# Optimization experiments

Measured on AMD Instinct MI355X. Metric: run time of the kernel, lower is better.

The kernel has to match this reference:

```python
import jax, jax.numpy as jnp
import numpy as np
from jax import lax


def _box_conv3d(x, win):
    k = jnp.ones((1, 1, win, win, win), x.dtype) / float(win ** 3)
    pad = win // 2
    return lax.conv_general_dilated(
        x, k,
        window_strides=(1, 1, 1),
        padding=[(pad, pad)] * 3,
        dimension_numbers=('NCDHW', 'OIDHW', 'NCDHW'),
    )


def setup_inputs() -> dict:
    key = jax.random.key(0)
    k1, k2 = jax.random.split(key)
    shape = (1, 1, 160, 192, 224)
    pred = jax.random.uniform(k1, shape, dtype=jnp.float32)
    target = jax.random.uniform(k2, shape, dtype=jnp.float32)
    return {'pred': pred, 'target': target, 'window_size': 9}


def reference(pred, target, window_size):
    Ii = target
    Ji = pred
    win = window_size
    mu1 = _box_conv3d(Ii, win)
    mu2 = _box_conv3d(Ji, win)
    mu1_sq = mu1 * mu1
    mu2_sq = mu2 * mu2
    mu1_mu2 = mu1 * mu2
    sigma1_sq = _box_conv3d(Ii * Ii, win) - mu1_sq
    sigma2_sq = _box_conv3d(Ji * Ji, win) - mu2_sq
    sigma12 = _box_conv3d(Ii * Ji, win) - mu1_mu2
    eps = jnp.finfo(sigma12.dtype).eps
    cc = sigma12 * sigma12 / jnp.maximum(sigma1_sq * sigma2_sq, eps)
    return -jnp.mean(cc)
```

## Files before the change

kernel.cpp:

```cpp
#include <hip/hip_runtime.h>
#include <hip/hip_fp16.h>

#define D_  160
#define H_  192
#define W_  224
#define HW_ (H_ * W_)
#define HW2_ (HW_ / 2)
#define N_  (D_ * H_ * W_)
#define INV729 (1.0f / 729.0f)
#define HSEG 16
#define NSEG (H_ / HSEG)
#define NROW (HSEG + 9)
#define UPD  (NSEG * 2)


__device__ __forceinline__ unsigned pack2(float a, float b) {
    const __half2 h = __floats2half2_rn(a, b);
    return *(const unsigned*)&h;
}

__global__ __launch_bounds__(64) void k_passWH(const float* __restrict__ pred,
                                               const float* __restrict__ targ,
                                               uint4* __restrict__ outA,
                                               unsigned* __restrict__ outB,
                                               double* __restrict__ acc) {
    if (blockIdx.x == 0 && threadIdx.x == 0) *acc = 0.0;

    const int lane = threadIdx.x;
    const int unit = blockIdx.x;
    const int d    = unit / UPD;
    const int rem  = unit % UPD;
    const int half = rem & 1;
    const int h0   = (rem >> 1) * HSEG;
    const long dbase = (long)d * HW_;
    const int wbase = half * 112;
    const int w0    = wbase + 2 * lane;

    if (lane < 56) {
        int coff[5];
        #pragma unroll
        for (int m = 0; m < 5; ++m) {
            const int wc = w0 - 4 + 2 * m;
            coff[m] = wc < 0 ? 0 : (wc > W_ - 2 ? W_ - 2 : wc);
        }
        bool vm[10];
        #pragma unroll
        for (int k = 0; k < 10; ++k) {
            const int wk = w0 - 4 + k;
            vm[k] = (wk >= 0) && (wk < W_);
        }

        float2 q[5][9];
        #pragma unroll
        for (int c = 0; c < 5; ++c)
            #pragma unroll
            for (int k = 0; k < 9; ++k) q[c][k] = make_float2(0.f, 0.f);
        float S0[5] = {0,0,0,0,0}, S1[5] = {0,0,0,0,0};

        const float* baseI = targ + dbase;
        const float* baseJ = pred + dbase;

        #pragma unroll
        for (int p = 0; p < NROW; ++p) {
            const int hh = h0 - 5 + p;
            float x[10], y[10];
            if (hh >= 0 && hh < H_) {
                const float* rI = baseI + (long)hh * W_;
                const float* rJ = baseJ + (long)hh * W_;
                #pragma unroll
                for (int m = 0; m < 5; ++m) {
                    const float2 vI = *(const float2*)(rI + coff[m]);
                    const float2 vJ = *(const float2*)(rJ + coff[m]);
                    x[2*m] = vI.x; x[2*m+1] = vI.y;
                    y[2*m] = vJ.x; y[2*m+1] = vJ.y;
                }
                #pragma unroll
                for (int k = 0; k < 10; ++k) {
                    if (k != 4 && k != 5) {
                        x[k] = vm[k] ? x[k] : 0.f;
                        y[k] = vm[k] ? y[k] : 0.f;
                    }
                }
            } else {
                #pragma unroll
                for (int k = 0; k < 10; ++k) { x[k] = 0.f; y[k] = 0.f; }
            }

            float sI = 0.f, sJ = 0.f, sII = 0.f, sJJ = 0.f, sIJ = 0.f;
            #pragma unroll
            for (int kk = 0; kk < 9; ++kk) {
                sI  += x[kk];          sJ  += y[kk];
                sII = fmaf(x[kk], x[kk], sII);
                sJJ = fmaf(y[kk], y[kk], sJJ);
                sIJ = fmaf(x[kk], y[kk], sIJ);
            }
            float w0s[5], w1s[5];
            w0s[0] = sI;  w1s[0] = sI  + x[9] - x[0];
            w0s[1] = sJ;  w1s[1] = sJ  + y[9] - y[0];
            w0s[2] = sII; w1s[2] = sII + x[9]*x[9] - x[0]*x[0];
            w0s[3] = sJJ; w1s[3] = sJJ + y[9]*y[9] - y[0]*y[0];
            w0s[4] = sIJ; w1s[4] = sIJ + x[9]*y[9] - x[0]*y[0];

            const int ph = p % 9;
            #pragma unroll
            for (int c = 0; c < 5; ++c) {
                S0[c] += w0s[c] - q[c][ph].x;
                S1[c] += w1s[c] - q[c][ph].y;
                q[c][ph].x = w0s[c];
                q[c][ph].y = w1s[c];
            }
            if (p >= 9) {
                const long rb = dbase + (long)(h0 + p - 9) * W_;
                uint4 oA;
                oA.x = pack2(S0[0], S0[1]); oA.y = pack2(S0[2], S0[3]);
                oA.z = pack2(S1[0], S1[1]); oA.w = pack2(S1[2], S1[3]);
                outA[rb / 2 + half * 56 + lane] = oA;
                outB[rb / 2 + half * 56 + lane] = pack2(S0[4], S1[4]);
            }
        }
    }
}

__global__ __launch_bounds__(256) void k_passD(const uint4* __restrict__ bufA,
                                               const unsigned* __restrict__ bufB,
                                               double* __restrict__ acc) {
    const int DSEG = D_ / 8;
    const int p2 = blockIdx.x * blockDim.x + threadIdx.x;
    const int d0 = blockIdx.y * DSEG;

    float2 q[5][9], S[5];
    #pragma unroll
    for (int c = 0; c < 5; ++c) S[c] = make_float2(0.f, 0.f);

    #pragma unroll
    for (int k = 0; k < 9; ++k) {
        const int dd = d0 - 5 + k;
        uint4 va = make_uint4(0u, 0u, 0u, 0u);
        unsigned vb = 0u;
        if (dd >= 0) {
            va = bufA[(long)dd * HW2_ + p2];
            vb = bufB[(long)dd * HW2_ + p2];
        }
        const float2 a01 = __half22float2(*(const __half2*)&va.x);
        const float2 a23 = __half22float2(*(const __half2*)&va.y);
        const float2 b01 = __half22float2(*(const __half2*)&va.z);
        const float2 b23 = __half22float2(*(const __half2*)&va.w);
        const float2 c44 = __half22float2(*(const __half2*)&vb);
        q[0][k] = make_float2(a01.x, b01.x); S[0].x += a01.x; S[0].y += b01.x;
        q[1][k] = make_float2(a01.y, b01.y); S[1].x += a01.y; S[1].y += b01.y;
        q[2][k] = make_float2(a23.x, b23.x); S[2].x += a23.x; S[2].y += b23.x;
        q[3][k] = make_float2(a23.y, b23.y); S[3].x += a23.y; S[3].y += b23.y;
        q[4][k] = make_float2(c44.x, c44.y); S[4].x += c44.x; S[4].y += c44.y;
    }

    float myacc = 0.f;
    #pragma unroll
    for (int j = 0; j < DSEG; ++j) {
        const int dd = d0 + 4 + j;
        uint4 va = make_uint4(0u, 0u, 0u, 0u);
        unsigned vb = 0u;
        if (dd < D_) {
            va = bufA[(long)dd * HW2_ + p2];
            vb = bufB[(long)dd * HW2_ + p2];
        }
        const float2 a01 = __half22float2(*(const __half2*)&va.x);
        const float2 a23 = __half22float2(*(const __half2*)&va.y);
        const float2 b01 = __half22float2(*(const __half2*)&va.z);
        const float2 b23 = __half22float2(*(const __half2*)&va.w);
        const float2 c44 = __half22float2(*(const __half2*)&vb);
        const float2 nv[5] = {
            make_float2(a01.x, b01.x), make_float2(a01.y, b01.y),
            make_float2(a23.x, b23.x), make_float2(a23.y, b23.y),
            make_float2(c44.x, c44.y)
        };
        const int ph = j % 9;
        #pragma unroll
        for (int c = 0; c < 5; ++c) {
            S[c].x += nv[c].x - q[c][ph].x;
            S[c].y += nv[c].y - q[c][ph].y;
            q[c][ph] = nv[c];
        }
        #pragma unroll
        for (int e = 0; e < 2; ++e) {
            const float mu1 = (e ? S[0].y : S[0].x) * INV729;
            const float mu2 = (e ? S[1].y : S[1].x) * INV729;
            const float s1  = (e ? S[2].y : S[2].x) * INV729 - mu1 * mu1;
            const float s2  = (e ? S[3].y : S[3].x) * INV729 - mu2 * mu2;
            const float s12 = (e ? S[4].y : S[4].x) * INV729 - mu1 * mu2;
            const float den = fmaxf(s1 * s2, 1.1920929e-7f);
            myacc += (s12 * s12) / den;
        }
    }

    __shared__ float red[256];
    red[threadIdx.x] = myacc;
    __syncthreads();
    #pragma unroll
    for (int s = 128; s > 0; s >>= 1) {
        if (threadIdx.x < s) red[threadIdx.x] += red[threadIdx.x + s];
        __syncthreads();
    }
    if (threadIdx.x == 0) atomicAdd(acc, (double)red[0]);
}

__global__ void k_fin(const double* __restrict__ acc, float* __restrict__ out) {
    out[0] = (float)(-(*acc) / (double)N_);
}

extern "C" void kernel_launch(void* const* d_in, const int* in_sizes, int n_in,
                              void* d_out, int out_size, void* d_ws, size_t ws_size,
                              hipStream_t stream) {
    const float* pred = (const float*)d_in[0];
    const float* targ = (const float*)d_in[1];

    uint4*    bufA = (uint4*)d_ws;
    unsigned* bufB = (unsigned*)((char*)d_ws + (size_t)(N_ / 2) * 16);
    double*   acc  = (double*)((char*)d_ws + (size_t)(N_ / 2) * 16 + (size_t)(N_ / 2) * 4);
    float*    out  = (float*)d_out;

    k_passWH<<<D_ * UPD, 64, 0, stream>>>(pred, targ, bufA, bufB, acc);
    dim3 g3(HW2_ / 256, 8);
    k_passD<<<g3, 256, 0, stream>>>(bufA, bufB, acc);
    k_fin<<<1, 1, 0, stream>>>(acc, out);
}
```

Baseline: 62.23 us.

## Split fused W/H box-filter pass into separate W and H kernels

Result: slower. 73.96 us (+18.8%).

```diff
diff --git a/kernel.cpp b/kernel.cpp
--- a/kernel.cpp
+++ b/kernel.cpp
@@ -7,11 +7,8 @@
 #define HW_ (H_ * W_)
 #define HW2_ (HW_ / 2)
 #define N_  (D_ * H_ * W_)
+#define NP2 (N_ / 2)
 #define INV729 (1.0f / 729.0f)
-#define HSEG 16
-#define NSEG (H_ / HSEG)
-#define NROW (HSEG + 9)
-#define UPD  (NSEG * 2)
 
 
 __device__ __forceinline__ unsigned pack2(float a, float b) {
@@ -19,105 +16,127 @@
     return *(const unsigned*)&h;
 }
 
-__global__ __launch_bounds__(64) void k_passWH(const float* __restrict__ pred,
+__global__ __launch_bounds__(256) void k_passW(const float* __restrict__ pred,
                                                const float* __restrict__ targ,
                                                uint4* __restrict__ outA,
                                                unsigned* __restrict__ outB,
                                                double* __restrict__ acc) {
     if (blockIdx.x == 0 && threadIdx.x == 0) *acc = 0.0;
-
-    const int lane = threadIdx.x;
-    const int unit = blockIdx.x;
-    const int d    = unit / UPD;
-    const int rem  = unit % UPD;
-    const int half = rem & 1;
-    const int h0   = (rem >> 1) * HSEG;
-    const long dbase = (long)d * HW_;
-    const int wbase = half * 112;
-    const int w0    = wbase + 2 * lane;
-
-    if (lane < 56) {
-        int coff[5];
+    const int pp = blockIdx.x * 256 + threadIdx.x;
+    const int row = pp / 112;
+    const int ri  = pp % 112;
+    const int w0  = 2 * ri;
+    const float* rI = targ + (long)row * W_;
+    const float* rJ = pred + (long)row * W_;
+
+    float x[10], y[10];
+    #pragma unroll
+    for (int m = 0; m < 5; ++m) {
+        const int wc  = w0 - 4 + 2 * m;
+        const int wcc = wc < 0 ? 0 : (wc > W_ - 2 ? W_ - 2 : wc);
+        const float2 vI = *(const float2*)(rI + wcc);
+        const float2 vJ = *(const float2*)(rJ + wcc);
+        x[2*m] = vI.x; x[2*m+1] = vI.y;
+        y[2*m] = vJ.x; y[2*m+1] = vJ.y;
+    }
+    #pragma unroll
+    for (int k = 0; k < 10; ++k) {
+        if (k != 4 && k != 5) {
+            const int wk = w0 - 4 + k;
+            const bool v = (wk >= 0) && (wk < W_);
+            x[k] = v ? x[k] : 0.f;
+            y[k] = v ? y[k] : 0.f;
+        }
+    }
+    float sI = 0.f, sJ = 0.f, sII = 0.f, sJJ = 0.f, sIJ = 0.f;
+    #pragma unroll
+    for (int kk = 0; kk < 9; ++kk) {
+        sI += x[kk]; sJ += y[kk];
+        sII = fmaf(x[kk], x[kk], sII);
+        sJJ = fmaf(y[kk], y[kk], sJJ);
+        sIJ = fmaf(x[kk], y[kk], sIJ);
+    }
+    const float tI  = sI  + x[9] - x[0];
+    const float tJ  = sJ  + y[9] - y[0];
+    const float tII = sII + x[9]*x[9] - x[0]*x[0];
+    const float tJJ = sJJ + y[9]*y[9] - y[0]*y[0];
+    const float tIJ = sIJ + x[9]*y[9] - x[0]*y[0];
+
+    uint4 oA;
+    oA.x = pack2(sI, sJ);  oA.y = pack2(sII, sJJ);
+    oA.z = pack2(tI, tJ);  oA.w = pack2(tII, tJJ);
+    outA[pp] = oA;
+    outB[pp] = pack2(sIJ, tIJ);
+}
+
+__global__ __launch_bounds__(256) void k_passH2(const uint4* __restrict__ inA,
+                                                const unsigned* __restrict__ inB,
+                                                uint4* __restrict__ outA,
+                                                unsigned* __restrict__ outB) {
+    const int HSEG2 = H_ / 8;
+    const int cc = blockIdx.x * blockDim.x + threadIdx.x;
+    const int d  = cc / 112;
+    const int ri = cc % 112;
+    const int h0 = blockIdx.y * HSEG2;
+    const long colbase = (long)d * HW2_ + ri;
+
+    float2 q[5][9], S[5];
+    #pragma unroll
+    for (int c = 0; c < 5; ++c) S[c] = make_float2(0.f, 0.f);
+
+    #pragma unroll
+    for (int k = 0; k < 9; ++k) {
+        const int hh = h0 - 5 + k;
+        uint4 va = make_uint4(0u, 0u, 0u, 0u);
+        unsigned vb = 0u;
+        if (hh >= 0) {
+            va = inA[colbase + (long)hh * 112];
+            vb = inB[colbase + (long)hh * 112];
+        }
+        const float2 f01 = __half22float2(*(const __half2*)&va.x);
+        const float2 f23 = __half22float2(*(const __half2*)&va.y);
+        const float2 g01 = __half22float2(*(const __half2*)&va.z);
+        const float2 g23 = __half22float2(*(const __half2*)&va.w);
+        const float2 c44 = __half22float2(*(const __half2*)&vb);
+        q[0][k] = make_float2(f01.x, g01.x); S[0].x += f01.x; S[0].y += g01.x;
+        q[1][k] = make_float2(f01.y, g01.y); S[1].x += f01.y; S[1].y += g01.y;
+        q[2][k] = make_float2(f23.x, g23.x); S[2].x += f23.x; S[2].y += g23.x;
+        q[3][k] = make_float2(f23.y, g23.y); S[3].x += f23.y; S[3].y += g23.y;
+        q[4][k] = make_float2(c44.x, c44.y); S[4].x += c44.x; S[4].y += c44.y;
+    }
+
+    #pragma unroll
+    for (int j = 0; j < HSEG2; ++j) {
+        const int hh = h0 + 4 + j;
+        uint4 va = make_uint4(0u, 0u, 0u, 0u);
+        unsigned vb = 0u;
+        if (hh < H_) {
+            va = inA[colbase + (long)hh * 112];
+            vb = inB[colbase + (long)hh * 112];
+        }
+        const float2 f01 = __half22float2(*(const __half2*)&va.x);
+        const float2 f23 = __half22float2(*(const __half2*)&va.y);
+        const float2 g01 = __half22float2(*(const __half2*)&va.z);
+        const float2 g23 = __half22float2(*(const __half2*)&va.w);
+        const float2 c44 = __half22float2(*(const __half2*)&vb);
+        const float2 nv[5] = {
+            make_float2(f01.x, g01.x), make_float2(f01.y, g01.y),
+            make_float2(f23.x, g23.x), make_float2(f23.y, g23.y),
+            make_float2(c44.x, c44.y)
+        };
+        const int ph = j % 9;
         #pragma unroll
-        for (int m = 0; m < 5; ++m) {
-            const int wc = w0 - 4 + 2 * m;
-            coff[m] = wc < 0 ? 0 : (wc > W_ - 2 ? W_ - 2 : wc);
-        }
-        bool vm[10];
-        #pragma unroll
-        for (int k = 0; k < 10; ++k) {
-            const int wk = w0 - 4 + k;
-            vm[k] = (wk >= 0) && (wk < W_);
-        }
-
-        float2 q[5][9];
-        #pragma unroll
-        for (int c = 0; c < 5; ++c)
-            #pragma unroll
-            for (int k = 0; k < 9; ++k) q[c][k] = make_float2(0.f, 0.f);
-        float S0[5] = {0,0,0,0,0}, S1[5] = {0,0,0,0,0};
-
-        const float* baseI = targ + dbase;
-        const float* baseJ = pred + dbase;
-
-        #pragma unroll
-        for (int p = 0; p < NROW; ++p) {
-            const int hh = h0 - 5 + p;
-            float x[10], y[10];
-            if (hh >= 0 && hh < H_) {
-                const float* rI = baseI + (long)hh * W_;
-                const float* rJ = baseJ + (long)hh * W_;
-                #pragma unroll
-                for (int m = 0; m < 5; ++m) {
-                    const float2 vI = *(const float2*)(rI + coff[m]);
-                    const float2 vJ = *(const float2*)(rJ + coff[m]);
-                    x[2*m] = vI.x; x[2*m+1] = vI.y;
-                    y[2*m] = vJ.x; y[2*m+1] = vJ.y;
-                }
-                #pragma unroll
-                for (int k = 0; k < 10; ++k) {
-                    if (k != 4 && k != 5) {
-                        x[k] = vm[k] ? x[k] : 0.f;
-                        y[k] = vm[k] ? y[k] : 0.f;
-                    }
-                }
-            } else {
-                #pragma unroll
-                for (int k = 0; k < 10; ++k) { x[k] = 0.f; y[k] = 0.f; }
-            }
-
-            float sI = 0.f, sJ = 0.f, sII = 0.f, sJJ = 0.f, sIJ = 0.f;
-            #pragma unroll
-            for (int kk = 0; kk < 9; ++kk) {
-                sI  += x[kk];          sJ  += y[kk];
-                sII = fmaf(x[kk], x[kk], sII);
-                sJJ = fmaf(y[kk], y[kk], sJJ);
-                sIJ = fmaf(x[kk], y[kk], sIJ);
-            }
-            float w0s[5], w1s[5];
-            w0s[0] = sI;  w1s[0] = sI  + x[9] - x[0];
-            w0s[1] = sJ;  w1s[1] = sJ  + y[9] - y[0];
-            w0s[2] = sII; w1s[2] = sII + x[9]*x[9] - x[0]*x[0];
-            w0s[3] = sJJ; w1s[3] = sJJ + y[9]*y[9] - y[0]*y[0];
-            w0s[4] = sIJ; w1s[4] = sIJ + x[9]*y[9] - x[0]*y[0];
-
-            const int ph = p % 9;
-            #pragma unroll
-            for (int c = 0; c < 5; ++c) {
-                S0[c] += w0s[c] - q[c][ph].x;
-                S1[c] += w1s[c] - q[c][ph].y;
-                q[c][ph].x = w0s[c];
-                q[c][ph].y = w1s[c];
-            }
-            if (p >= 9) {
-                const long rb = dbase + (long)(h0 + p - 9) * W_;
-                uint4 oA;
-                oA.x = pack2(S0[0], S0[1]); oA.y = pack2(S0[2], S0[3]);
-                oA.z = pack2(S1[0], S1[1]); oA.w = pack2(S1[2], S1[3]);
-                outA[rb / 2 + half * 56 + lane] = oA;
-                outB[rb / 2 + half * 56 + lane] = pack2(S0[4], S1[4]);
-            }
-        }
+        for (int c = 0; c < 5; ++c) {
+            S[c].x += nv[c].x - q[c][ph].x;
+            S[c].y += nv[c].y - q[c][ph].y;
+            q[c][ph] = nv[c];
+        }
+        const long op = colbase + (long)(h0 + j) * 112;
+        uint4 oA;
+        oA.x = pack2(S[0].x, S[1].x); oA.y = pack2(S[2].x, S[3].x);
+        oA.z = pack2(S[0].y, S[1].y); oA.w = pack2(S[2].y, S[3].y);
+        outA[op] = oA;
+        outB[op] = pack2(S[4].x, S[4].y);
     }
 }
 
@@ -213,13 +232,18 @@
     const float* pred = (const float*)d_in[0];
     const float* targ = (const float*)d_in[1];
 
-    uint4*    bufA = (uint4*)d_ws;
-    unsigned* bufB = (unsigned*)((char*)d_ws + (size_t)(N_ / 2) * 16);
-    double*   acc  = (double*)((char*)d_ws + (size_t)(N_ / 2) * 16 + (size_t)(N_ / 2) * 4);
-    float*    out  = (float*)d_out;
-
-    k_passWH<<<D_ * UPD, 64, 0, stream>>>(pred, targ, bufA, bufB, acc);
+    char* ws = (char*)d_ws;
+    uint4*    bufA1 = (uint4*)ws;
+    unsigned* bufB1 = (unsigned*)(ws + (size_t)NP2 * 16);
+    uint4*    bufA2 = (uint4*)(ws + (size_t)NP2 * 20);
+    unsigned* bufB2 = (unsigned*)(ws + (size_t)NP2 * 36);
+    double*   acc   = (double*)(ws + (size_t)NP2 * 40);
+    float*    out   = (float*)d_out;
+
+    k_passW<<<NP2 / 256, 256, 0, stream>>>(pred, targ, bufA1, bufB1, acc);
+    dim3 g2(17920 / 256, 8);
+    k_passH2<<<g2, 256, 0, stream>>>(bufA1, bufB1, bufA2, bufB2);
     dim3 g3(HW2_ / 256, 8);
-    k_passD<<<g3, 256, 0, stream>>>(bufA, bufB, acc);
+    k_passD<<<g3, 256, 0, stream>>>(bufA2, bufB2, acc);
     k_fin<<<1, 1, 0, stream>>>(acc, out);
 }
```
